# Kernel tuning notes

Measured on AMD Instinct MI355X. Metric: run time of the kernel, lower is better.

The kernel has to match this reference:

```python
import jax, jax.numpy as jnp
import numpy as np

H = 16  # num_heads


def setup_inputs() -> dict:
    key = jax.random.key(0)
    k1, k2, k3, k4, k5 = jax.random.split(key, 5)
    B, T, C = 4, 2048, 1024
    s = 1.0 / np.sqrt(C)
    return {
        "x": jax.random.normal(k1, (B, T, C), dtype=jnp.float32),
        "W_attn": jax.random.normal(k2, (C, 3 * C), dtype=jnp.float32) * s,
        "b_attn": jax.random.normal(k3, (3 * C,), dtype=jnp.float32) * 0.02,
        "W_proj": jax.random.normal(k4, (C, C), dtype=jnp.float32) * s,
        "b_proj": jax.random.normal(k5, (C,), dtype=jnp.float32) * 0.02,
    }


def reference(x, W_attn, b_attn, W_proj, b_proj):
    B, T, C = x.shape
    hd = C // H  # head_dim
    qkv = x @ W_attn + b_attn                      # [B,T,3C]
    q, k, v = jnp.split(qkv, 3, axis=-1)
    # [B,T,C] -> [B,H,T,hd]
    q = q.reshape(B, T, H, hd).transpose(0, 2, 1, 3)
    k = k.reshape(B, T, H, hd).transpose(0, 2, 1, 3)
    v = v.reshape(B, T, H, hd).transpose(0, 2, 1, 3)
    att = jnp.einsum("bhqd,bhkd->bhqk", q, k) * (1.0 / np.sqrt(hd))
    causal = jnp.tril(jnp.ones((T, T), dtype=bool))
    att = jnp.where(causal[None, None], att, -jnp.inf)
    att = jax.nn.softmax(att, axis=-1)
    y = jnp.einsum("bhqk,bhkd->bhqd", att, v)      # [B,H,T,hd]
    y = y.transpose(0, 2, 1, 3).reshape(B, T, C)
    return y @ W_proj + b_proj
```

## Files before the change

kernel.cpp:

```cpp
#include <hip/hip_runtime.h>
#include <hip/hip_bf16.h>

typedef float  f32x4 __attribute__((ext_vector_type(4)));
typedef short  s16x8 __attribute__((ext_vector_type(8)));
typedef unsigned short u16x4 __attribute__((ext_vector_type(4)));
typedef __bf16 bfv8  __attribute__((ext_vector_type(8)));
typedef __bf16 bfv2  __attribute__((ext_vector_type(2)));

__device__ __forceinline__ f32x4 MFMA(s16x8 a, s16x8 b, f32x4 c) {
  return __builtin_amdgcn_mfma_f32_16x16x32_bf16(
      __builtin_bit_cast(bfv8, a), __builtin_bit_cast(bfv8, b), c, 0, 0, 0);
}

#define GLDS16(gp, lp) __builtin_amdgcn_global_load_lds( \
    (const __attribute__((address_space(1))) void*)(gp), \
    (__attribute__((address_space(3))) void*)(lp), 16, 0, 0)

__device__ __forceinline__ unsigned short f2bf(float f) {
  unsigned int u = __builtin_bit_cast(unsigned int, f);
  u += 0x7fffu + ((u >> 16) & 1u);
  return (unsigned short)(u >> 16);
}

__device__ __forceinline__ unsigned pk2(float a, float b) {
  bfv2 t; t[0] = (__bf16)a; t[1] = (__bf16)b;
  return __builtin_bit_cast(unsigned, t);
}

__global__ __launch_bounds__(256) void cvt_bf16(const float* __restrict__ in,
                                                short* __restrict__ out, int n) {
  int i = (blockIdx.x * 256 + threadIdx.x) * 4;
  if (i >= n) return;
  float4 v = *(const float4*)(in + i);
  u16x4 o;
  o[0] = f2bf(v.x); o[1] = f2bf(v.y); o[2] = f2bf(v.z); o[3] = f2bf(v.w);
  *(u16x4*)(out + i) = o;
}

__global__ __launch_bounds__(1024) void transpose_cvt(const float* __restrict__ W,
                                                      short* __restrict__ WT,
                                                      int rows, int cols) {
  __shared__ float tile[32][33];
  const int tx = threadIdx.x, ty = threadIdx.y;
  tile[ty][tx] = W[(size_t)(blockIdx.y * 32 + ty) * cols + blockIdx.x * 32 + tx];
  __syncthreads();
  const int nrow = blockIdx.x * 32 + ty;
  const int kcol = blockIdx.y * 32 + tx;
  WT[(size_t)nrow * rows + kcol] = (short)f2bf(tile[tx][ty]);
}

template<int MODE>
__global__ __launch_bounds__(256) void gemm_bt(
    const short* __restrict__ A, const short* __restrict__ Bm,
    const float* __restrict__ bias,
    short* __restrict__ q_out, short* __restrict__ k_out, short* __restrict__ v_out,
    float* __restrict__ f_out, int K) {
  __shared__ short Abuf[2][128 * 32];
  __shared__ short Bbuf[2][128 * 32];
  const int bn = blockIdx.x, bm = blockIdx.y;
  const int tid = threadIdx.x, wid = tid >> 6, lane = tid & 63;
  const int wr = wid >> 1, wc = wid & 1;
  const int c = lane & 15, g = lane >> 4;

  f32x4 acc[4][4];
#pragma unroll
  for (int m = 0; m < 4; m++)
#pragma unroll
    for (int n = 0; n < 4; n++) acc[m][n] = (f32x4)0.f;

  const int r0 = wid * 32 + (lane >> 2);
  const int ch0 = (lane & 3) ^ (r0 & 3);
  const short* Ag = A + (size_t)(bm * 128 + r0) * K + ch0 * 8;
  const short* Bg = Bm + (size_t)(bn * 128 + r0) * K + ch0 * 8;
  const size_t rowstep = (size_t)16 * K;

  auto STAGE = [&](int b, int k0) {
    GLDS16(Ag + k0,           (char*)Abuf[b] + wid * 2048);
    GLDS16(Ag + rowstep + k0, (char*)Abuf[b] + wid * 2048 + 1024);
    GLDS16(Bg + k0,           (char*)Bbuf[b] + wid * 2048);
    GLDS16(Bg + rowstep + k0, (char*)Bbuf[b] + wid * 2048 + 1024);
  };

  STAGE(0, 0);
  int cur = 0;
  for (int k0 = 0; k0 < K; k0 += 32) {
    __syncthreads();
    if (k0 + 32 < K) STAGE(cur ^ 1, k0 + 32);
    s16x8 af[4], bfr[4];
#pragma unroll
    for (int m = 0; m < 4; m++) {
      int row = wr * 64 + m * 16 + c;
      af[m] = *(const s16x8*)((const char*)Abuf[cur] + row * 64 + ((g ^ (row & 3)) * 16));
    }
#pragma unroll
    for (int n = 0; n < 4; n++) {
      int row = wc * 64 + n * 16 + c;
      bfr[n] = *(const s16x8*)((const char*)Bbuf[cur] + row * 64 + ((g ^ (row & 3)) * 16));
    }
#pragma unroll
    for (int m = 0; m < 4; m++)
#pragma unroll
      for (int n = 0; n < 4; n++) acc[m][n] = MFMA(af[m], bfr[n], acc[m][n]);
    cur ^= 1;
  }

  const int featbase = bm * 128 + wr * 64;
  const int tokbase = bn * 128 + wc * 64;
#pragma unroll
  for (int m = 0; m < 4; m++) {
    const int f0 = featbase + m * 16 + 4 * g;
    float b4[4];
#pragma unroll
    for (int r = 0; r < 4; r++) b4[r] = bias[f0 + r];
    if (MODE == 0) {
      const int sect = f0 >> 10;
      const int fin = f0 & 1023;
      const int h = fin >> 6, d0 = fin & 63;
#pragma unroll
      for (int n = 0; n < 4; n++) {
        const int token = tokbase + n * 16 + c;
        const int b = token >> 11, t = token & 2047;
        const f32x4 v = acc[m][n];
        if (sect == 0) {
          u16x4 o;
#pragma unroll
          for (int r = 0; r < 4; r++) o[r] = f2bf((v[r] + b4[r]) * 0.125f);
          *(u16x4*)(q_out + ((size_t)((b * 16 + h) * 2048 + t)) * 64 + d0) = o;
        } else if (sect == 1) {
          u16x4 o;
#pragma unroll
          for (int r = 0; r < 4; r++) o[r] = f2bf(v[r] + b4[r]);
          *(u16x4*)(k_out + ((size_t)((b * 16 + h) * 2048 + t)) * 64 + d0) = o;
        } else {
#pragma unroll
          for (int r = 0; r < 4; r++)
            v_out[((size_t)((b * 16 + h) * 64 + d0 + r)) * 2048 + t] = (short)f2bf(v[r] + b4[r]);
        }
      }
    } else {
#pragma unroll
      for (int n = 0; n < 4; n++) {
        const int token = tokbase + n * 16 + c;
        f32x4 o = acc[m][n];
#pragma unroll
        for (int r = 0; r < 4; r++) o[r] += b4[r];
        *(f32x4*)(f_out + (size_t)token * 1024 + f0) = o;
      }
    }
  }
}

__global__ __launch_bounds__(256, 4) void attn_fused(
    const short* __restrict__ Qg, const short* __restrict__ Kg,
    const short* __restrict__ Vtg, short* __restrict__ Yg) {
  __shared__ short K_lds[2 * 4096];
  __shared__ short Vt_lds[2 * 4096];
  __shared__ short P_lds[4096];
  const int id = blockIdx.x;
  const int virt = (id & 7) * 128 + (id >> 3);
  const int bh = virt >> 4, pp = virt & 15;
  const int NT = 32 - pp;
  const int q0lo = pp * 64, q0hi = (31 - pp) * 64;
  const int tid = threadIdx.x, wid = tid >> 6, lane = tid & 63;
  const int c = lane & 15, g = lane >> 4;

  const short* Qb = Qg + (size_t)bh * (2048 * 64);
  const short* Kb = Kg + (size_t)bh * (2048 * 64);
  const short* Vb = Vtg + (size_t)bh * (64 * 2048);

  s16x8 qlo[2], qhi[2];
  {
    const short* qp = Qb + (size_t)(q0lo + wid * 16 + c) * 64 + 8 * g;
    qlo[0] = *(const s16x8*)qp;
    qlo[1] = *(const s16x8*)(qp + 32);
    qp = Qb + (size_t)(q0hi + wid * 16 + c) * 64 + 8 * g;
    qhi[0] = *(const s16x8*)qp;
    qhi[1] = *(const s16x8*)(qp + 32);
  }

  f32x4 acc_lo[4], acc_hi[4];
#pragma unroll
  for (int jd = 0; jd < 4; jd++) { acc_lo[jd] = (f32x4)0.f; acc_hi[jd] = (f32x4)0.f; }
  float l_lo = 0.f, l_hi = 0.f;

  const int srow = wid * 16 + (lane >> 3);
  const int sch = lane & 7;
  char* Pw = (char*)P_lds + wid * 2048;

  auto STAGE = [&](int b, int kt) {
#pragma unroll
    for (int cc = 0; cc < 2; ++cc) {
      const int row = srow + cc * 8;
      const int ch = sch ^ (row & 7);
      GLDS16(Kb + (size_t)(kt * 64 + row) * 64 + ch * 8,
             (char*)K_lds + b * 8192 + wid * 2048 + cc * 1024);
      GLDS16(Vb + (size_t)row * 2048 + kt * 64 + ch * 8,
             (char*)Vt_lds + b * 8192 + wid * 2048 + cc * 1024);
    }
  };

  auto SOFTMAX_PV = [&](f32x4* sa, bool diag, f32x4* acc, float& l, const char* Vl) {
    float lp = 0.f;
#pragma unroll
    for (int jm = 0; jm < 4; jm++) {
      float e[4];
#pragma unroll
      for (int r = 0; r < 4; r++) {
        float sv = sa[jm][r];
        if (diag && (jm * 16 + 4 * g + r > wid * 16 + c)) sv = -1e30f;
        e[r] = __expf(sv);
        lp += e[r];
      }
      uint2 w;
      w.x = pk2(e[0], e[1]);
      w.y = pk2(e[2], e[3]);
      *(uint2*)(Pw + c * 128 + (((2 * jm + (g >> 1)) ^ (c & 7)) * 16) + (g & 1) * 8) = w;
    }
    l += lp;
    asm volatile("" ::: "memory");
    s16x8 pf[2];
#pragma unroll
    for (int ks = 0; ks < 2; ks++)
      pf[ks] = *(const s16x8*)(Pw + c * 128 + (((4 * ks + g) ^ (c & 7)) * 16));
#pragma unroll
    for (int jd = 0; jd < 4; jd++) {
      const int row = jd * 16 + c, sw = row & 7;
#pragma unroll
      for (int ks = 0; ks < 2; ks++) {
        s16x8 vf = *(const s16x8*)(Vl + row * 128 + (((4 * ks + g) ^ sw) * 16));
        acc[jd] = MFMA(vf, pf[ks], acc[jd]);
      }
    }
  };

  STAGE(0, 0);
  for (int kt = 0; kt < NT; ++kt) {
    __syncthreads();
    if (kt + 1 < NT) STAGE((kt + 1) & 1, kt + 1);
    const char* Kl = (const char*)K_lds + (kt & 1) * 8192;
    const char* Vl = (const char*)Vt_lds + (kt & 1) * 8192;
    const bool lo_act = (kt <= pp);

    f32x4 sh[4], sl[4];
#pragma unroll
    for (int jm = 0; jm < 4; jm++) { sh[jm] = (f32x4)0.f; sl[jm] = (f32x4)0.f; }
#pragma unroll
    for (int jm = 0; jm < 4; jm++) {
      const int row = jm * 16 + c, sw = row & 7;
#pragma unroll
      for (int ks = 0; ks < 2; ks++) {
        s16x8 kf = *(const s16x8*)(Kl + row * 128 + (((4 * ks + g) ^ sw) * 16));
        sh[jm] = MFMA(kf, qhi[ks], sh[jm]);
        if (lo_act) sl[jm] = MFMA(kf, qlo[ks], sl[jm]);
      }
    }
    SOFTMAX_PV(sh, kt == NT - 1, acc_hi, l_hi, Vl);
    if (lo_act) SOFTMAX_PV(sl, kt == pp, acc_lo, l_lo, Vl);
  }

  l_hi += __shfl_xor(l_hi, 16); l_hi += __shfl_xor(l_hi, 32);
  l_lo += __shfl_xor(l_lo, 16); l_lo += __shfl_xor(l_lo, 32);

  auto WRITE_Y = [&](const f32x4* acc, float l, int q0) {
    const float inv = 1.f / l;
    const size_t yrow =
        (size_t)((bh >> 4) * 2048 + q0 + wid * 16 + c) * 1024 + (bh & 15) * 64;
#pragma unroll
    for (int jd = 0; jd < 4; jd++) {
      u16x4 o;
#pragma unroll
      for (int r = 0; r < 4; r++) o[r] = f2bf(acc[jd][r] * inv);
      *(u16x4*)(Yg + yrow + jd * 16 + 4 * g) = o;
    }
  };
  WRITE_Y(acc_hi, l_hi, q0hi);
  WRITE_Y(acc_lo, l_lo, q0lo);
}

extern "C" void kernel_launch(void* const* d_in, const int* in_sizes, int n_in,
                              void* d_out, int out_size, void* d_ws, size_t ws_size,
                              hipStream_t stream) {
  (void)in_sizes; (void)n_in; (void)out_size;
  const float* x      = (const float*)d_in[0];
  const float* W_attn = (const float*)d_in[1];
  const float* b_attn = (const float*)d_in[2];
  const float* W_proj = (const float*)d_in[3];
  const float* b_proj = (const float*)d_in[4];
  float* out = (float*)d_out;
  char* ws = (char*)d_ws;
  if (ws_size < 92274688u) return;

  short* xb  = (short*)(ws);
  short* waT = (short*)(ws + 16777216);
  short* wpT = (short*)(ws + 23068672);
  short* qb_ = (short*)(ws + 25165824);
  short* kb_ = (short*)(ws + 41943040);
  short* vb_ = (short*)(ws + 58720256);
  short* yb_ = (short*)(ws + 75497472);

  cvt_bf16<<<8192, 256, 0, stream>>>(x, xb, 8388608);
  transpose_cvt<<<dim3(96, 32), dim3(32, 32), 0, stream>>>(W_attn, waT, 1024, 3072);
  transpose_cvt<<<dim3(32, 32), dim3(32, 32), 0, stream>>>(W_proj, wpT, 1024, 1024);
  gemm_bt<0><<<dim3(64, 24), 256, 0, stream>>>(waT, xb, b_attn, qb_, kb_, vb_, nullptr, 1024);
  attn_fused<<<1024, 256, 0, stream>>>(qb_, kb_, vb_, yb_);
  gemm_bt<1><<<dim3(64, 8), 256, 0, stream>>>(wpT, yb_, b_proj, nullptr, nullptr, nullptr, out, 1024);
}
```

Before: 265.3 us.

## Replace QKV GEMM with 256x256-tile 8-wave kernel using 4-stage LDS pipeline

Swaps the QKV projection GEMM for a dedicated kernel that uses 256x256 output tiles, 512 threads (8 waves), a 4-deep global-to-LDS prefetch ring with explicit vmcnt waits, split A/B staging interleaved with MFMA bursts, s_setprio around the MFMA bursts, and an XCD-aware block remap. The aim is more data reuse per LDS load and better hiding of memory latency behind MFMA work. The output projection keeps the old 128-tile kernel, now specialised. In exchange it uses 128KB of LDS per block at one block per CU, and the 384 blocks may leave some CUs idle in the tail.

```diff
diff --git a/kernel.cpp b/kernel.cpp
--- a/kernel.cpp
+++ b/kernel.cpp
@@ -49,12 +49,135 @@
   WT[(size_t)nrow * rows + kcol] = (short)f2bf(tile[tx][ty]);
 }
 
-template<int MODE>
-__global__ __launch_bounds__(256) void gemm_bt(
+__global__ __launch_bounds__(512, 1) void gemm_qkv8p(
     const short* __restrict__ A, const short* __restrict__ Bm,
     const float* __restrict__ bias,
-    short* __restrict__ q_out, short* __restrict__ k_out, short* __restrict__ v_out,
-    float* __restrict__ f_out, int K) {
+    short* __restrict__ q_out, short* __restrict__ k_out, short* __restrict__ v_out) {
+  __shared__ short As[4][8192];
+  __shared__ short Bs[4][8192];
+
+  const int id = blockIdx.x;
+  const int vid = (id & 7) * 48 + (id >> 3);
+  const int bm = vid >> 5, bn = vid & 31;
+  const int tid = threadIdx.x, wid = tid >> 6, lane = tid & 63;
+  const int wm = wid >> 2, wn = wid & 3;
+  const int c = lane & 15, g = lane >> 4;
+
+  const short* Ag = A + (size_t)(bm * 256) * 1024;
+  const short* Bg = Bm + (size_t)(bn * 256) * 1024;
+
+  f32x4 acc[8][4];
+#pragma unroll
+  for (int mi = 0; mi < 8; ++mi)
+#pragma unroll
+    for (int ni = 0; ni < 4; ++ni) acc[mi][ni] = (f32x4)0.f;
+
+  auto STAGE_A = [&](int sl) {
+    const int k0 = sl * 32;
+    char* dst = (char*)As[sl & 3];
+#pragma unroll
+    for (int j = 0; j < 2; ++j) {
+      const int row = j * 128 + (tid >> 2);
+      const int ch = (tid & 3) ^ ((row >> 1) & 3);
+      GLDS16(Ag + (size_t)row * 1024 + k0 + ch * 8, dst + j * 8192 + wid * 1024);
+    }
+  };
+  auto STAGE_B = [&](int sl) {
+    const int k0 = sl * 32;
+    char* dst = (char*)Bs[sl & 3];
+#pragma unroll
+    for (int j = 0; j < 2; ++j) {
+      const int row = j * 128 + (tid >> 2);
+      const int ch = (tid & 3) ^ ((row >> 1) & 3);
+      GLDS16(Bg + (size_t)row * 1024 + k0 + ch * 8, dst + j * 8192 + wid * 1024);
+    }
+  };
+  auto LD = [&](const char* base, int row) -> s16x8 {
+    return *(const s16x8*)(base + row * 64 + ((g ^ ((row >> 1) & 3)) * 16));
+  };
+
+  STAGE_A(0); STAGE_B(0);
+  STAGE_A(1); STAGE_B(1);
+  STAGE_A(2); STAGE_B(2);
+  asm volatile("s_waitcnt vmcnt(8)" ::: "memory");
+  __builtin_amdgcn_s_barrier();
+
+  for (int s = 0; s < 32; ++s) {
+    const char* Asl = (const char*)As[s & 3];
+    const char* Bsl = (const char*)Bs[s & 3];
+    const int sl3 = s + 3;
+    s16x8 a8[8];
+#pragma unroll
+    for (int mi = 0; mi < 8; ++mi) a8[mi] = LD(Asl, wm * 128 + mi * 16 + c);
+    s16x8 b0 = LD(Bsl, wn * 64 + c);
+    s16x8 b1 = LD(Bsl, wn * 64 + 16 + c);
+    if (sl3 < 32) STAGE_A(sl3);
+    __builtin_amdgcn_s_barrier();
+    asm volatile("s_waitcnt lgkmcnt(0)" ::: "memory");
+    __builtin_amdgcn_sched_barrier(0);
+    __builtin_amdgcn_s_setprio(1);
+#pragma unroll
+    for (int mi = 0; mi < 8; ++mi) acc[mi][0] = MFMA(a8[mi], b0, acc[mi][0]);
+#pragma unroll
+    for (int mi = 0; mi < 8; ++mi) acc[mi][1] = MFMA(a8[mi], b1, acc[mi][1]);
+    __builtin_amdgcn_s_setprio(0);
+    __builtin_amdgcn_s_barrier();
+    s16x8 b2 = LD(Bsl, wn * 64 + 32 + c);
+    s16x8 b3 = LD(Bsl, wn * 64 + 48 + c);
+    if (sl3 < 32) STAGE_B(sl3);
+    __builtin_amdgcn_s_barrier();
+    asm volatile("s_waitcnt lgkmcnt(0)" ::: "memory");
+    __builtin_amdgcn_sched_barrier(0);
+    __builtin_amdgcn_s_setprio(1);
+#pragma unroll
+    for (int mi = 0; mi < 8; ++mi) acc[mi][2] = MFMA(a8[mi], b2, acc[mi][2]);
+#pragma unroll
+    for (int mi = 0; mi < 8; ++mi) acc[mi][3] = MFMA(a8[mi], b3, acc[mi][3]);
+    __builtin_amdgcn_s_setprio(0);
+    if (s <= 28)      asm volatile("s_waitcnt vmcnt(8)" ::: "memory");
+    else if (s == 29) asm volatile("s_waitcnt vmcnt(4)" ::: "memory");
+    else              asm volatile("s_waitcnt vmcnt(0)" ::: "memory");
+    __builtin_amdgcn_s_barrier();
+  }
+
+  const int featbase = bm * 256 + wm * 128;
+  const int tokbase = bn * 256 + wn * 64;
+  const int sect = featbase >> 10;
+#pragma unroll
+  for (int mi = 0; mi < 8; ++mi) {
+    const int f0 = featbase + mi * 16 + 4 * g;
+    float b4[4];
+#pragma unroll
+    for (int r = 0; r < 4; ++r) b4[r] = bias[f0 + r];
+    const int fin = f0 & 1023;
+    const int h = fin >> 6, d0 = fin & 63;
+#pragma unroll
+    for (int ni = 0; ni < 4; ++ni) {
+      const int token = tokbase + ni * 16 + c;
+      const int b = token >> 11, t = token & 2047;
+      const f32x4 v = acc[mi][ni];
+      if (sect == 0) {
+        u16x4 o;
+#pragma unroll
+        for (int r = 0; r < 4; ++r) o[r] = f2bf((v[r] + b4[r]) * 0.125f);
+        *(u16x4*)(q_out + ((size_t)((b * 16 + h) * 2048 + t)) * 64 + d0) = o;
+      } else if (sect == 1) {
+        u16x4 o;
+#pragma unroll
+        for (int r = 0; r < 4; ++r) o[r] = f2bf(v[r] + b4[r]);
+        *(u16x4*)(k_out + ((size_t)((b * 16 + h) * 2048 + t)) * 64 + d0) = o;
+      } else {
+#pragma unroll
+        for (int r = 0; r < 4; ++r)
+          v_out[((size_t)((b * 16 + h) * 64 + d0 + r)) * 2048 + t] = (short)f2bf(v[r] + b4[r]);
+      }
+    }
+  }
+}
+
+__global__ __launch_bounds__(256) void gemm_proj(
+    const short* __restrict__ A, const short* __restrict__ Bm,
+    const float* __restrict__ bias, float* __restrict__ f_out, int K) {
   __shared__ short Abuf[2][128 * 32];
   __shared__ short Bbuf[2][128 * 32];
   const int bn = blockIdx.x, bm = blockIdx.y;
@@ -112,40 +235,13 @@
     float b4[4];
 #pragma unroll
     for (int r = 0; r < 4; r++) b4[r] = bias[f0 + r];
-    if (MODE == 0) {
-      const int sect = f0 >> 10;
-      const int fin = f0 & 1023;
-      const int h = fin >> 6, d0 = fin & 63;
-#pragma unroll
-      for (int n = 0; n < 4; n++) {
-        const int token = tokbase + n * 16 + c;
-        const int b = token >> 11, t = token & 2047;
-        const f32x4 v = acc[m][n];
-        if (sect == 0) {
-          u16x4 o;
-#pragma unroll
-          for (int r = 0; r < 4; r++) o[r] = f2bf((v[r] + b4[r]) * 0.125f);
-          *(u16x4*)(q_out + ((size_t)((b * 16 + h) * 2048 + t)) * 64 + d0) = o;
-        } else if (sect == 1) {
-          u16x4 o;
-#pragma unroll
-          for (int r = 0; r < 4; r++) o[r] = f2bf(v[r] + b4[r]);
-          *(u16x4*)(k_out + ((size_t)((b * 16 + h) * 2048 + t)) * 64 + d0) = o;
-        } else {
-#pragma unroll
-          for (int r = 0; r < 4; r++)
-            v_out[((size_t)((b * 16 + h) * 64 + d0 + r)) * 2048 + t] = (short)f2bf(v[r] + b4[r]);
-        }
-      }
-    } else {
-#pragma unroll
-      for (int n = 0; n < 4; n++) {
-        const int token = tokbase + n * 16 + c;
-        f32x4 o = acc[m][n];
-#pragma unroll
-        for (int r = 0; r < 4; r++) o[r] += b4[r];
-        *(f32x4*)(f_out + (size_t)token * 1024 + f0) = o;
-      }
+#pragma unroll
+    for (int n = 0; n < 4; n++) {
+      const int token = tokbase + n * 16 + c;
+      f32x4 o = acc[m][n];
+#pragma unroll
+      for (int r = 0; r < 4; r++) o[r] += b4[r];
+      *(f32x4*)(f_out + (size_t)token * 1024 + f0) = o;
     }
   }
 }
@@ -301,7 +397,7 @@
   cvt_bf16<<<8192, 256, 0, stream>>>(x, xb, 8388608);
   transpose_cvt<<<dim3(96, 32), dim3(32, 32), 0, stream>>>(W_attn, waT, 1024, 3072);
   transpose_cvt<<<dim3(32, 32), dim3(32, 32), 0, stream>>>(W_proj, wpT, 1024, 1024);
-  gemm_bt<0><<<dim3(64, 24), 256, 0, stream>>>(waT, xb, b_attn, qb_, kb_, vb_, nullptr, 1024);
+  gemm_qkv8p<<<384, 512, 0, stream>>>(waT, xb, b_attn, qb_, kb_, vb_);
   attn_fused<<<1024, 256, 0, stream>>>(qb_, kb_, vb_, yb_);
-  gemm_bt<1><<<dim3(64, 8), 256, 0, stream>>>(wpT, yb_, b_proj, nullptr, nullptr, nullptr, out, 1024);
-}
+  gemm_proj<<<dim3(64, 8), 256, 0, stream>>>(wpT, yb_, b_proj, out, 1024);
+}
```

Result: slower. 273.1 us (+3.0%).
